# Kernel optimization log

Measured on AMD Instinct MI355X. Metric: run time of the kernel, lower is better.

## Reference

```python
import jax, jax.numpy as jnp
import numpy as np

EMB = 256
HEADS = 8

def setup_inputs() -> dict:
    key = jax.random.key(0)
    k1, k2, k3, k4, k5 = jax.random.split(key, 5)
    b, t = 8, 1024
    scale = 1.0 / np.sqrt(EMB)
    x = jax.random.normal(k1, (b, t, EMB), dtype=jnp.float32)
    # nn.Linear weights stored as [out, in]; we store [in, out] for x @ W
    Wk = jax.random.normal(k2, (EMB, EMB * HEADS), dtype=jnp.float32) * scale
    Wq = jax.random.normal(k3, (EMB, EMB * HEADS), dtype=jnp.float32) * scale
    Wv = jax.random.normal(k4, (EMB, EMB * HEADS), dtype=jnp.float32) * scale
    Wu = jax.random.normal(k5, (EMB * HEADS, EMB), dtype=jnp.float32) * scale
    return {"x": x, "Wq": Wq, "Wk": Wk, "Wv": Wv, "Wu": Wu}

def reference(x, Wq, Wk, Wv, Wu):
    b, t, e = x.shape
    h, d = HEADS, EMB  # per-head dim equals emb_in in this module
    q = (x @ Wq).reshape(b, t, h, d)
    k = (x @ Wk).reshape(b, t, h, d)
    v = (x @ Wv).reshape(b, t, h, d)
    inv4 = d ** (-0.25)
    q = q * inv4
    k = k * inv4
    # scores: [b, h, t, t]
    dot = jnp.einsum('bthd,bshd->bhts', q, k)
    attn = jax.nn.softmax(dot, axis=-1)
    out = jnp.einsum('bhts,bshd->bthd', attn, v).reshape(b, t, h * d)
    return out @ Wu
```

## Files before the change

### kernel.cpp

```cpp
#include <hip/hip_runtime.h>
#include <stdint.h>

typedef unsigned short u16;
typedef __bf16 bf16x8 __attribute__((ext_vector_type(8)));
typedef float f32x4 __attribute__((ext_vector_type(4)));
typedef u16 u16x8 __attribute__((ext_vector_type(8)));

#define MFMA16(a, b, c) __builtin_amdgcn_mfma_f32_16x16x32_bf16((a), (b), (c), 0, 0, 0)

__device__ __forceinline__ u16 f2bf(float f) {
  union { float f; uint32_t u; } v; v.f = f;
  uint32_t u = v.u;
  return (u16)((u + 0x7FFFu + ((u >> 16) & 1u)) >> 16);
}

__device__ __forceinline__ uint32_t pk2(float a, float b) {
  union { __bf16 h[2]; uint32_t u; } v;
  v.h[0] = (__bf16)a; v.h[1] = (__bf16)b;
  return v.u;
}

__device__ __forceinline__ void gload_lds16(const u16* g, u16* l) {
  __builtin_amdgcn_global_load_lds((const __attribute__((address_space(1))) void*)g,
                                   (__attribute__((address_space(3))) void*)l, 16, 0, 0);
}

__global__ void cvt_bf16(const float* __restrict__ in, u16* __restrict__ out, int n4) {
  int i = blockIdx.x * 256 + threadIdx.x;
  if (i < n4) {
    float4 v = ((const float4*)in)[i];
    ushort4 o;
    o.x = f2bf(v.x); o.y = f2bf(v.y); o.z = f2bf(v.z); o.w = f2bf(v.w);
    ((ushort4*)out)[i] = o;
  }
}

__global__ __launch_bounds__(256) void transpose_cvt(const float* __restrict__ in,
                                                     u16* __restrict__ out,
                                                     int R, int C, float scale) {
  __shared__ float t32[32][33];
  int c0 = blockIdx.x * 32, r0 = blockIdx.y * 32;
  int tx = threadIdx.x & 31, ty = threadIdx.x >> 5;
  #pragma unroll
  for (int i = 0; i < 32; i += 8)
    t32[ty + i][tx] = in[(size_t)(r0 + ty + i) * C + c0 + tx] * scale;
  __syncthreads();
  #pragma unroll
  for (int i = 0; i < 32; i += 8)
    out[(size_t)(c0 + ty + i) * R + r0 + tx] = f2bf(t32[tx][ty + i]);
}

template<int FOUT>
__global__ __launch_bounds__(256, 2) void gemm_bt(const u16* __restrict__ A,
                                                  const u16* __restrict__ Bt,
                                                  void* __restrict__ Cout,
                                                  int M, int N, int K,
                                                  int lda, int ldb, int ldc) {
  __shared__ __attribute__((aligned(16))) u16 As[128 * 32];
  __shared__ __attribute__((aligned(16))) u16 Bs[128 * 32];
  const int tid = threadIdx.x;
  const int lane = tid & 63;
  const int w = tid >> 6;
  const int wr = w >> 1, wc = w & 1;
  const int row0 = blockIdx.y * 128, col0 = blockIdx.x * 128;
  const int rr = lane & 15, kg = lane >> 4;

  f32x4 acc[4][4];
  const f32x4 fz = {0.f, 0.f, 0.f, 0.f};
  #pragma unroll
  for (int m = 0; m < 4; ++m)
    #pragma unroll
    for (int n = 0; n < 4; ++n) acc[m][n] = fz;

  for (int k0 = 0; k0 < K; k0 += 32) {
    #pragma unroll
    for (int c = 0; c < 2; ++c) {
      int Lb = c * 256 + w * 64;
      int L = Lb + lane;
      int r = L >> 2, cc = L & 3;
      gload_lds16(&A[(size_t)(row0 + r) * lda + k0 + cc * 8], &As[Lb << 3]);
      gload_lds16(&Bt[(size_t)(col0 + r) * ldb + k0 + cc * 8], &Bs[Lb << 3]);
    }
    __syncthreads();
    bf16x8 af[4], bfr[4];
    #pragma unroll
    for (int m = 0; m < 4; ++m)
      af[m] = *(const bf16x8*)&As[(wr * 64 + m * 16 + rr) * 32 + kg * 8];
    #pragma unroll
    for (int n = 0; n < 4; ++n)
      bfr[n] = *(const bf16x8*)&Bs[(wc * 64 + n * 16 + rr) * 32 + kg * 8];
    #pragma unroll
    for (int m = 0; m < 4; ++m)
      #pragma unroll
      for (int n = 0; n < 4; ++n)
        acc[m][n] = MFMA16(af[m], bfr[n], acc[m][n]);
    __syncthreads();
  }

  #pragma unroll
  for (int m = 0; m < 4; ++m)
    #pragma unroll
    for (int n = 0; n < 4; ++n) {
      int r = row0 + wr * 64 + m * 16 + kg * 4;
      int c = col0 + wc * 64 + n * 16 + rr;
      if (FOUT == 2) {
        int bb = r >> 10, tt = r & 1023;
        int hh = c >> 8, dd = c & 255;
        union { u16 h4[4]; uint2 u2; } o4;
        #pragma unroll
        for (int j = 0; j < 4; ++j) o4.h4[j] = f2bf(acc[m][n][j]);
        *(uint2*)&((u16*)Cout)[(size_t)(bb * 8 + hh) * 262144 + (size_t)dd * 1024 + tt] = o4.u2;
      } else {
        #pragma unroll
        for (int j = 0; j < 4; ++j) {
          if (FOUT == 0)
            ((u16*)Cout)[(size_t)(r + j) * ldc + c] = f2bf(acc[m][n][j]);
          else
            ((float*)Cout)[(size_t)(r + j) * ldc + c] = acc[m][n][j];
        }
      }
    }
}

template<int FOUT>
__global__ __launch_bounds__(256, 2) void gemm_bt64(const u16* __restrict__ A,
                                                    const u16* __restrict__ Bt,
                                                    void* __restrict__ Cout,
                                                    int M, int N, int K,
                                                    int lda, int ldb, int ldc) {
  __shared__ __attribute__((aligned(16))) u16 As[64 * 32];
  __shared__ __attribute__((aligned(16))) u16 Bs[128 * 32];
  const int tid = threadIdx.x;
  const int lane = tid & 63;
  const int w = tid >> 6;
  const int row0 = blockIdx.y * 64, col0 = blockIdx.x * 128;
  const int rr = lane & 15, kg = lane >> 4;

  f32x4 acc[4][2];
  const f32x4 fz = {0.f, 0.f, 0.f, 0.f};
  #pragma unroll
  for (int m = 0; m < 4; ++m)
    #pragma unroll
    for (int n = 0; n < 2; ++n) acc[m][n] = fz;

  for (int k0 = 0; k0 < K; k0 += 32) {
    {
      int Lb = w * 64;
      int L = Lb + lane;
      int r = L >> 2, cc = L & 3;
      gload_lds16(&A[(size_t)(row0 + r) * lda + k0 + cc * 8], &As[Lb << 3]);
    }
    #pragma unroll
    for (int c = 0; c < 2; ++c) {
      int Lb = c * 256 + w * 64;
      int L = Lb + lane;
      int r = L >> 2, cc = L & 3;
      gload_lds16(&Bt[(size_t)(col0 + r) * ldb + k0 + cc * 8], &Bs[Lb << 3]);
    }
    __syncthreads();
    bf16x8 af[4], bfr[2];
    #pragma unroll
    for (int m = 0; m < 4; ++m)
      af[m] = *(const bf16x8*)&As[(m * 16 + rr) * 32 + kg * 8];
    #pragma unroll
    for (int n = 0; n < 2; ++n)
      bfr[n] = *(const bf16x8*)&Bs[(w * 32 + n * 16 + rr) * 32 + kg * 8];
    #pragma unroll
    for (int m = 0; m < 4; ++m)
      #pragma unroll
      for (int n = 0; n < 2; ++n)
        acc[m][n] = MFMA16(af[m], bfr[n], acc[m][n]);
    __syncthreads();
  }

  #pragma unroll
  for (int m = 0; m < 4; ++m)
    #pragma unroll
    for (int n = 0; n < 2; ++n) {
      int r = row0 + m * 16 + kg * 4;
      int c = col0 + w * 32 + n * 16 + rr;
      #pragma unroll
      for (int j = 0; j < 4; ++j) {
        if (FOUT == 0)
          ((u16*)Cout)[(size_t)(r + j) * ldc + c] = f2bf(acc[m][n][j]);
        else
          ((float*)Cout)[(size_t)(r + j) * ldc + c] = acc[m][n][j];
      }
    }
}

__global__ __launch_bounds__(512) void attn_kernel(const u16* __restrict__ Q,
                                                   const u16* __restrict__ Kg,
                                                   const u16* __restrict__ Vt,
                                                   u16* __restrict__ O) {
  __shared__ __attribute__((aligned(16))) u16 smem[65536];
  u16* Ks = smem;
  u16* Vs = smem + 32768;
  const int tid = threadIdx.x;
  const int lane = tid & 63;
  const int w = tid >> 6;
  const int rr = lane & 15, kg = lane >> 4;
  const int bid = blockIdx.x;
  const int swz = (bid & 7) * 64 + (bid >> 3);
  const int bh = swz >> 3;
  const int b = bh >> 3, h = bh & 7;
  const int q0 = (swz & 7) * 128;
  const u16* Qb = Q + (size_t)b * 1024 * 2048 + (size_t)h * 256;
  const u16* Kb = Kg + (size_t)b * 1024 * 2048 + (size_t)h * 256;
  const u16* Vb = Vt + (size_t)bh * 262144;
  u16* Ob = O + (size_t)b * 1024 * 2048 + (size_t)h * 256;
  const int qrow = q0 + w * 16 + rr;

  auto stage_kv = [&](int sb, int s0i) {
    u16* Kd = Ks + sb * 16384;
    u16* Vd = Vs + sb * 16384;
    #pragma unroll
    for (int c = 0; c < 4; ++c) {
      int Lb = (c * 8 + w) * 64;
      int L = Lb + lane;
      int r = L >> 5, cc = L & 31;
      gload_lds16(&Kb[(size_t)(s0i + r) * 2048 + ((cc ^ (r & 7)) << 3)], &Kd[Lb << 3]);
      int rv = L >> 3, cv = L & 7;
      gload_lds16(&Vb[(size_t)rv * 1024 + s0i + ((cv ^ (rv & 7)) << 3)], &Vd[Lb << 3]);
    }
  };

  stage_kv(0, 0);

  bf16x8 qf[8];
  {
    const u16* qp = Qb + (size_t)qrow * 2048;
    #pragma unroll
    for (int kk = 0; kk < 8; ++kk) qf[kk] = *(const bf16x8*)&qp[kk * 32 + kg * 8];
  }

  const f32x4 fz = {0.f, 0.f, 0.f, 0.f};
  f32x4 oacc[16];
  #pragma unroll
  for (int dt = 0; dt < 16; ++dt) oacc[dt] = fz;
  float mrow = -1e30f, lrow = 0.f;

  __syncthreads();

  int buf = 0;
  for (int t = 0; t < 16; ++t) {
    if (t < 15) stage_kv(buf ^ 1, (t + 1) * 64);

    const u16* Kd = Ks + buf * 16384;
    f32x4 sacc[4];
    #pragma unroll
    for (int n4 = 0; n4 < 4; ++n4) sacc[n4] = fz;
    __builtin_amdgcn_s_setprio(1);
    #pragma unroll
    for (int kk = 0; kk < 8; ++kk) {
      #pragma unroll
      for (int n4 = 0; n4 < 4; ++n4) {
        int row = n4 * 16 + rr;
        int ck = kk * 4 + kg;
        bf16x8 kf = *(const bf16x8*)&Kd[row * 256 + ((ck ^ (row & 7)) << 3)];
        sacc[n4] = MFMA16(kf, qf[kk], sacc[n4]);
      }
    }
    __builtin_amdgcn_s_setprio(0);

    float vmax = sacc[0][0];
    #pragma unroll
    for (int n4 = 0; n4 < 4; ++n4)
      #pragma unroll
      for (int j = 0; j < 4; ++j) vmax = fmaxf(vmax, sacc[n4][j]);
    vmax = fmaxf(vmax, __shfl_xor(vmax, 16, 64));
    vmax = fmaxf(vmax, __shfl_xor(vmax, 32, 64));
    if (__any(vmax > mrow + 8.f)) {
      float mn = fmaxf(mrow, vmax);
      float resc = __expf(mrow - mn);
      mrow = mn;
      lrow *= resc;
      #pragma unroll
      for (int dt = 0; dt < 16; ++dt)
        #pragma unroll
        for (int i = 0; i < 4; ++i) oacc[dt][i] *= resc;
    }
    float sum = 0.f;
    uint32_t L0, H0, L1, H1, L2, H2, L3, H3;
    {
      float e0, e1, e2, e3;
      e0 = __expf(sacc[0][0] - mrow); e1 = __expf(sacc[0][1] - mrow);
      e2 = __expf(sacc[0][2] - mrow); e3 = __expf(sacc[0][3] - mrow);
      sum += (e0 + e1) + (e2 + e3); L0 = pk2(e0, e1); H0 = pk2(e2, e3);
      e0 = __expf(sacc[1][0] - mrow); e1 = __expf(sacc[1][1] - mrow);
      e2 = __expf(sacc[1][2] - mrow); e3 = __expf(sacc[1][3] - mrow);
      sum += (e0 + e1) + (e2 + e3); L1 = pk2(e0, e1); H1 = pk2(e2, e3);
      e0 = __expf(sacc[2][0] - mrow); e1 = __expf(sacc[2][1] - mrow);
      e2 = __expf(sacc[2][2] - mrow); e3 = __expf(sacc[2][3] - mrow);
      sum += (e0 + e1) + (e2 + e3); L2 = pk2(e0, e1); H2 = pk2(e2, e3);
      e0 = __expf(sacc[3][0] - mrow); e1 = __expf(sacc[3][1] - mrow);
      e2 = __expf(sacc[3][2] - mrow); e3 = __expf(sacc[3][3] - mrow);
      sum += (e0 + e1) + (e2 + e3); L3 = pk2(e0, e1); H3 = pk2(e2, e3);
    }
    sum += __shfl_xor(sum, 16, 64);
    sum += __shfl_xor(sum, 32, 64);
    lrow += sum;

    const u16* Vd = Vs + buf * 16384;
    const int g = kg;
    #pragma unroll
    for (int t2 = 0; t2 < 2; ++t2) {
      uint32_t La = t2 ? L2 : L0, Ha = t2 ? H2 : H0;
      uint32_t Lb2 = t2 ? L3 : L1, Hb = t2 ? H3 : H1;
      uint32_t La1 = __shfl_xor(La, 16, 64), La2 = __shfl_xor(La, 32, 64);
      uint32_t La3 = __shfl_xor(La1, 32, 64);
      uint32_t Ha1 = __shfl_xor(Ha, 16, 64), Ha2 = __shfl_xor(Ha, 32, 64);
      uint32_t Ha3 = __shfl_xor(Ha1, 32, 64);
      uint32_t Lb1 = __shfl_xor(Lb2, 16, 64), Lb2s = __shfl_xor(Lb2, 32, 64);
      uint32_t Lb3 = __shfl_xor(Lb1, 32, 64);
      uint32_t Hb1 = __shfl_xor(Hb, 16, 64), Hb2 = __shfl_xor(Hb, 32, 64);
      uint32_t Hb3 = __shfl_xor(Hb1, 32, 64);
      uint32_t a2S  = (g == 0) ? La  : (g == 1) ? La3 : (g == 2) ? La2 : La1;
      uint32_t a2S1 = (g == 0) ? La1 : (g == 1) ? La2 : (g == 2) ? La3 : La;
      uint32_t ah2S  = (g == 0) ? Ha  : (g == 1) ? Ha3 : (g == 2) ? Ha2 : Ha1;
      uint32_t ah2S1 = (g == 0) ? Ha1 : (g == 1) ? Ha2 : (g == 2) ? Ha3 : Ha;
      uint32_t b2S  = (g == 0) ? Lb2 : (g == 1) ? Lb3 : (g == 2) ? Lb2s : Lb1;
      uint32_t b2S1 = (g == 0) ? Lb1 : (g == 1) ? Lb2s : (g == 2) ? Lb3 : Lb2;
      uint32_t bh2S  = (g == 0) ? Hb  : (g == 1) ? Hb3 : (g == 2) ? Hb2 : Hb1;
      uint32_t bh2S1 = (g == 0) ? Hb1 : (g == 1) ? Hb2 : (g == 2) ? Hb3 : Hb;
      const int Qn = g >> 1;
      union { uint32_t u[4]; bf16x8 v; } pf;
      pf.u[0] = Qn ? b2S  : a2S;
      pf.u[1] = Qn ? bh2S : ah2S;
      pf.u[2] = Qn ? b2S1 : a2S1;
      pf.u[3] = Qn ? bh2S1 : ah2S1;
      __builtin_amdgcn_s_setprio(1);
      #pragma unroll
      for (int dt = 0; dt < 16; ++dt) {
        int rv = dt * 16 + rr;
        int cv = t2 * 4 + kg;
        bf16x8 vf = *(const bf16x8*)&Vd[rv * 64 + ((cv ^ (rv & 7)) << 3)];
        oacc[dt] = MFMA16(vf, pf.v, oacc[dt]);
      }
      __builtin_amdgcn_s_setprio(0);
    }

    __syncthreads();
    buf ^= 1;
  }

  float inv = 1.0f / lrow;
  #pragma unroll
  for (int dt = 0; dt < 16; ++dt) {
    union { u16 h4[4]; uint2 u2; } o4;
    #pragma unroll
    for (int i = 0; i < 4; ++i) o4.h4[i] = f2bf(oacc[dt][i] * inv);
    *(uint2*)&Ob[(size_t)qrow * 2048 + dt * 16 + kg * 4] = o4.u2;
  }
}

extern "C" void kernel_launch(void* const* d_in, const int* in_sizes, int n_in,
                              void* d_out, int out_size, void* d_ws, size_t ws_size,
                              hipStream_t stream) {
  const float* x  = (const float*)d_in[0];
  const float* Wq = (const float*)d_in[1];
  const float* Wk = (const float*)d_in[2];
  const float* Wv = (const float*)d_in[3];
  const float* Wu = (const float*)d_in[4];

  u16* xb  = (u16*)d_ws;
  u16* WtQ = xb  + 8192 * 256;
  u16* WtK = WtQ + 2048 * 256;
  u16* WtV = WtK + 2048 * 256;
  u16* Wut = WtV + 2048 * 256;
  u16* Qm  = Wut + 2048 * 256;
  u16* Km  = Qm  + (size_t)8192 * 2048;
  u16* Vtm = Km  + (size_t)8192 * 2048;
  u16* Om  = Vtm + (size_t)8192 * 2048;

  const float inv4 = 0.25f;

  cvt_bf16<<<2048, 256, 0, stream>>>(x, xb, 8192 * 256 / 4);
  transpose_cvt<<<dim3(64, 8), 256, 0, stream>>>(Wq, WtQ, 256, 2048, inv4);
  transpose_cvt<<<dim3(64, 8), 256, 0, stream>>>(Wk, WtK, 256, 2048, inv4);
  transpose_cvt<<<dim3(64, 8), 256, 0, stream>>>(Wv, WtV, 256, 2048, 1.0f);
  transpose_cvt<<<dim3(8, 64), 256, 0, stream>>>(Wu, Wut, 2048, 256, 1.0f);

  gemm_bt<0><<<dim3(16, 64), 256, 0, stream>>>(xb, WtQ, Qm, 8192, 2048, 256, 256, 256, 2048);
  gemm_bt<0><<<dim3(16, 64), 256, 0, stream>>>(xb, WtK, Km, 8192, 2048, 256, 256, 256, 2048);
  gemm_bt<2><<<dim3(16, 64), 256, 0, stream>>>(xb, WtV, Vtm, 8192, 2048, 256, 256, 256, 0);

  attn_kernel<<<512, 512, 0, stream>>>(Qm, Km, Vtm, Om);

  gemm_bt64<1><<<dim3(2, 128), 256, 0, stream>>>(Om, Wut, d_out, 8192, 256, 2048, 2048, 2048, 256);
}
```

Measured before the change: 215.1 us.

## Fuse QKV projections into one GEMM and process two query tiles per attention wave

The three Q/K/V projection GEMMs are merged into one launch over a concatenated 6144-column output. Each output tile routes to Q, K or the transposed V layout by column range, relying on WtQ, WtK and WtV sitting contiguously in the workspace. The attention kernel now gives each wave 32 query rows (two 16-row sets) instead of 16, so every K and V fragment read from LDS feeds two MFMAs, and the grid is halved to 256 blocks. This cuts LDS traffic and launch overhead per unit of work, but roughly doubles accumulator register use and halves the number of attention blocks, which may lower occupancy and leave CUs idle.

```diff
diff --git a/kernel.cpp b/kernel.cpp
--- a/kernel.cpp
+++ b/kernel.cpp
@@ -50,12 +50,11 @@
     out[(size_t)(c0 + ty + i) * R + r0 + tx] = f2bf(t32[tx][ty + i]);
 }
 
-template<int FOUT>
-__global__ __launch_bounds__(256, 2) void gemm_bt(const u16* __restrict__ A,
-                                                  const u16* __restrict__ Bt,
-                                                  void* __restrict__ Cout,
-                                                  int M, int N, int K,
-                                                  int lda, int ldb, int ldc) {
+__global__ __launch_bounds__(256, 2) void gemm_qkv(const u16* __restrict__ A,
+                                                   const u16* __restrict__ Bt,
+                                                   u16* __restrict__ Qm,
+                                                   u16* __restrict__ Km,
+                                                   u16* __restrict__ Vtm) {
   __shared__ __attribute__((aligned(16))) u16 As[128 * 32];
   __shared__ __attribute__((aligned(16))) u16 Bs[128 * 32];
   const int tid = threadIdx.x;
@@ -72,14 +71,14 @@
     #pragma unroll
     for (int n = 0; n < 4; ++n) acc[m][n] = fz;
 
-  for (int k0 = 0; k0 < K; k0 += 32) {
+  for (int k0 = 0; k0 < 256; k0 += 32) {
     #pragma unroll
     for (int c = 0; c < 2; ++c) {
       int Lb = c * 256 + w * 64;
       int L = Lb + lane;
       int r = L >> 2, cc = L & 3;
-      gload_lds16(&A[(size_t)(row0 + r) * lda + k0 + cc * 8], &As[Lb << 3]);
-      gload_lds16(&Bt[(size_t)(col0 + r) * ldb + k0 + cc * 8], &Bs[Lb << 3]);
+      gload_lds16(&A[(size_t)(row0 + r) * 256 + k0 + cc * 8], &As[Lb << 3]);
+      gload_lds16(&Bt[(size_t)(col0 + r) * 256 + k0 + cc * 8], &Bs[Lb << 3]);
     }
     __syncthreads();
     bf16x8 af[4], bfr[4];
@@ -103,21 +102,23 @@
     for (int n = 0; n < 4; ++n) {
       int r = row0 + wr * 64 + m * 16 + kg * 4;
       int c = col0 + wc * 64 + n * 16 + rr;
-      if (FOUT == 2) {
+      if (c < 2048) {
+        #pragma unroll
+        for (int j = 0; j < 4; ++j)
+          Qm[(size_t)(r + j) * 2048 + c] = f2bf(acc[m][n][j]);
+      } else if (c < 4096) {
+        int c2 = c - 2048;
+        #pragma unroll
+        for (int j = 0; j < 4; ++j)
+          Km[(size_t)(r + j) * 2048 + c2] = f2bf(acc[m][n][j]);
+      } else {
+        int c2 = c - 4096;
         int bb = r >> 10, tt = r & 1023;
-        int hh = c >> 8, dd = c & 255;
+        int hh = c2 >> 8, dd = c2 & 255;
         union { u16 h4[4]; uint2 u2; } o4;
         #pragma unroll
         for (int j = 0; j < 4; ++j) o4.h4[j] = f2bf(acc[m][n][j]);
-        *(uint2*)&((u16*)Cout)[(size_t)(bb * 8 + hh) * 262144 + (size_t)dd * 1024 + tt] = o4.u2;
-      } else {
-        #pragma unroll
-        for (int j = 0; j < 4; ++j) {
-          if (FOUT == 0)
-            ((u16*)Cout)[(size_t)(r + j) * ldc + c] = f2bf(acc[m][n][j]);
-          else
-            ((float*)Cout)[(size_t)(r + j) * ldc + c] = acc[m][n][j];
-        }
+        *(uint2*)&Vtm[(size_t)(bb * 8 + hh) * 262144 + (size_t)dd * 1024 + tt] = o4.u2;
       }
     }
 }
@@ -189,6 +190,49 @@
     }
 }
 
+struct PK8 { uint32_t L[4], H[4]; float sum; };
+
+__device__ __forceinline__ PK8 exppack(const f32x4* sacc, float m) {
+  PK8 r; r.sum = 0.f;
+  #pragma unroll
+  for (int n4 = 0; n4 < 4; ++n4) {
+    float e0 = __expf(sacc[n4][0] - m), e1 = __expf(sacc[n4][1] - m);
+    float e2 = __expf(sacc[n4][2] - m), e3 = __expf(sacc[n4][3] - m);
+    r.sum += (e0 + e1) + (e2 + e3);
+    r.L[n4] = pk2(e0, e1);
+    r.H[n4] = pk2(e2, e3);
+  }
+  return r;
+}
+
+__device__ __forceinline__ bf16x8 make_pf(const PK8& p, int t2, int g) {
+  uint32_t La = t2 ? p.L[2] : p.L[0], Ha = t2 ? p.H[2] : p.H[0];
+  uint32_t Lb2 = t2 ? p.L[3] : p.L[1], Hb = t2 ? p.H[3] : p.H[1];
+  uint32_t La1 = __shfl_xor(La, 16, 64), La2 = __shfl_xor(La, 32, 64);
+  uint32_t La3 = __shfl_xor(La1, 32, 64);
+  uint32_t Ha1 = __shfl_xor(Ha, 16, 64), Ha2 = __shfl_xor(Ha, 32, 64);
+  uint32_t Ha3 = __shfl_xor(Ha1, 32, 64);
+  uint32_t Lb1 = __shfl_xor(Lb2, 16, 64), Lb2s = __shfl_xor(Lb2, 32, 64);
+  uint32_t Lb3 = __shfl_xor(Lb1, 32, 64);
+  uint32_t Hb1 = __shfl_xor(Hb, 16, 64), Hb2 = __shfl_xor(Hb, 32, 64);
+  uint32_t Hb3 = __shfl_xor(Hb1, 32, 64);
+  uint32_t a2S  = (g == 0) ? La  : (g == 1) ? La3 : (g == 2) ? La2 : La1;
+  uint32_t a2S1 = (g == 0) ? La1 : (g == 1) ? La2 : (g == 2) ? La3 : La;
+  uint32_t ah2S  = (g == 0) ? Ha  : (g == 1) ? Ha3 : (g == 2) ? Ha2 : Ha1;
+  uint32_t ah2S1 = (g == 0) ? Ha1 : (g == 1) ? Ha2 : (g == 2) ? Ha3 : Ha;
+  uint32_t b2S  = (g == 0) ? Lb2 : (g == 1) ? Lb3 : (g == 2) ? Lb2s : Lb1;
+  uint32_t b2S1 = (g == 0) ? Lb1 : (g == 1) ? Lb2s : (g == 2) ? Lb3 : Lb2;
+  uint32_t bh2S  = (g == 0) ? Hb  : (g == 1) ? Hb3 : (g == 2) ? Hb2 : Hb1;
+  uint32_t bh2S1 = (g == 0) ? Hb1 : (g == 1) ? Hb2 : (g == 2) ? Hb3 : Hb;
+  const int Qn = g >> 1;
+  union { uint32_t u[4]; bf16x8 v; } pf;
+  pf.u[0] = Qn ? b2S : a2S;
+  pf.u[1] = Qn ? bh2S : ah2S;
+  pf.u[2] = Qn ? b2S1 : a2S1;
+  pf.u[3] = Qn ? bh2S1 : ah2S1;
+  return pf.v;
+}
+
 __global__ __launch_bounds__(512) void attn_kernel(const u16* __restrict__ Q,
                                                    const u16* __restrict__ Kg,
                                                    const u16* __restrict__ Vt,
@@ -201,15 +245,16 @@
   const int w = tid >> 6;
   const int rr = lane & 15, kg = lane >> 4;
   const int bid = blockIdx.x;
-  const int swz = (bid & 7) * 64 + (bid >> 3);
-  const int bh = swz >> 3;
+  const int swz = (bid & 7) * 32 + (bid >> 3);
+  const int bh = swz >> 2;
   const int b = bh >> 3, h = bh & 7;
-  const int q0 = (swz & 7) * 128;
+  const int q0 = (swz & 3) * 256;
   const u16* Qb = Q + (size_t)b * 1024 * 2048 + (size_t)h * 256;
   const u16* Kb = Kg + (size_t)b * 1024 * 2048 + (size_t)h * 256;
   const u16* Vb = Vt + (size_t)bh * 262144;
   u16* Ob = O + (size_t)b * 1024 * 2048 + (size_t)h * 256;
-  const int qrow = q0 + w * 16 + rr;
+  const int qrowA = q0 + w * 32 + rr;
+  const int qrowB = qrowA + 16;
 
   auto stage_kv = [&](int sb, int s0i) {
     u16* Kd = Ks + sb * 16384;
@@ -227,18 +272,22 @@
 
   stage_kv(0, 0);
 
-  bf16x8 qf[8];
+  bf16x8 qfA[8], qfB[8];
   {
-    const u16* qp = Qb + (size_t)qrow * 2048;
-    #pragma unroll
-    for (int kk = 0; kk < 8; ++kk) qf[kk] = *(const bf16x8*)&qp[kk * 32 + kg * 8];
+    const u16* qpA = Qb + (size_t)qrowA * 2048;
+    const u16* qpB = Qb + (size_t)qrowB * 2048;
+    #pragma unroll
+    for (int kk = 0; kk < 8; ++kk) {
+      qfA[kk] = *(const bf16x8*)&qpA[kk * 32 + kg * 8];
+      qfB[kk] = *(const bf16x8*)&qpB[kk * 32 + kg * 8];
+    }
   }
 
   const f32x4 fz = {0.f, 0.f, 0.f, 0.f};
-  f32x4 oacc[16];
-  #pragma unroll
-  for (int dt = 0; dt < 16; ++dt) oacc[dt] = fz;
-  float mrow = -1e30f, lrow = 0.f;
+  f32x4 oaccA[16], oaccB[16];
+  #pragma unroll
+  for (int dt = 0; dt < 16; ++dt) { oaccA[dt] = fz; oaccB[dt] = fz; }
+  float mrowA = -1e30f, lrowA = 0.f, mrowB = -1e30f, lrowB = 0.f;
 
   __syncthreads();
 
@@ -247,9 +296,9 @@
     if (t < 15) stage_kv(buf ^ 1, (t + 1) * 64);
 
     const u16* Kd = Ks + buf * 16384;
-    f32x4 sacc[4];
-    #pragma unroll
-    for (int n4 = 0; n4 < 4; ++n4) sacc[n4] = fz;
+    f32x4 saccA[4], saccB[4];
+    #pragma unroll
+    for (int n4 = 0; n4 < 4; ++n4) { saccA[n4] = fz; saccB[n4] = fz; }
     __builtin_amdgcn_s_setprio(1);
     #pragma unroll
     for (int kk = 0; kk < 8; ++kk) {
@@ -258,84 +307,57 @@
         int row = n4 * 16 + rr;
         int ck = kk * 4 + kg;
         bf16x8 kf = *(const bf16x8*)&Kd[row * 256 + ((ck ^ (row & 7)) << 3)];
-        sacc[n4] = MFMA16(kf, qf[kk], sacc[n4]);
+        saccA[n4] = MFMA16(kf, qfA[kk], saccA[n4]);
+        saccB[n4] = MFMA16(kf, qfB[kk], saccB[n4]);
       }
     }
     __builtin_amdgcn_s_setprio(0);
 
-    float vmax = sacc[0][0];
+    float vmaxA = saccA[0][0], vmaxB = saccB[0][0];
     #pragma unroll
     for (int n4 = 0; n4 < 4; ++n4)
       #pragma unroll
-      for (int j = 0; j < 4; ++j) vmax = fmaxf(vmax, sacc[n4][j]);
-    vmax = fmaxf(vmax, __shfl_xor(vmax, 16, 64));
-    vmax = fmaxf(vmax, __shfl_xor(vmax, 32, 64));
-    if (__any(vmax > mrow + 8.f)) {
-      float mn = fmaxf(mrow, vmax);
-      float resc = __expf(mrow - mn);
-      mrow = mn;
-      lrow *= resc;
+      for (int j = 0; j < 4; ++j) {
+        vmaxA = fmaxf(vmaxA, saccA[n4][j]);
+        vmaxB = fmaxf(vmaxB, saccB[n4][j]);
+      }
+    vmaxA = fmaxf(vmaxA, __shfl_xor(vmaxA, 16, 64));
+    vmaxA = fmaxf(vmaxA, __shfl_xor(vmaxA, 32, 64));
+    vmaxB = fmaxf(vmaxB, __shfl_xor(vmaxB, 16, 64));
+    vmaxB = fmaxf(vmaxB, __shfl_xor(vmaxB, 32, 64));
+    if (__any((vmaxA > mrowA + 8.f) || (vmaxB > mrowB + 8.f))) {
+      float mnA = fmaxf(mrowA, vmaxA), mnB = fmaxf(mrowB, vmaxB);
+      float rsA = __expf(mrowA - mnA), rsB = __expf(mrowB - mnB);
+      mrowA = mnA; mrowB = mnB;
+      lrowA *= rsA; lrowB *= rsB;
       #pragma unroll
       for (int dt = 0; dt < 16; ++dt)
         #pragma unroll
-        for (int i = 0; i < 4; ++i) oacc[dt][i] *= resc;
-    }
-    float sum = 0.f;
-    uint32_t L0, H0, L1, H1, L2, H2, L3, H3;
-    {
-      float e0, e1, e2, e3;
-      e0 = __expf(sacc[0][0] - mrow); e1 = __expf(sacc[0][1] - mrow);
-      e2 = __expf(sacc[0][2] - mrow); e3 = __expf(sacc[0][3] - mrow);
-      sum += (e0 + e1) + (e2 + e3); L0 = pk2(e0, e1); H0 = pk2(e2, e3);
-      e0 = __expf(sacc[1][0] - mrow); e1 = __expf(sacc[1][1] - mrow);
-      e2 = __expf(sacc[1][2] - mrow); e3 = __expf(sacc[1][3] - mrow);
-      sum += (e0 + e1) + (e2 + e3); L1 = pk2(e0, e1); H1 = pk2(e2, e3);
-      e0 = __expf(sacc[2][0] - mrow); e1 = __expf(sacc[2][1] - mrow);
-      e2 = __expf(sacc[2][2] - mrow); e3 = __expf(sacc[2][3] - mrow);
-      sum += (e0 + e1) + (e2 + e3); L2 = pk2(e0, e1); H2 = pk2(e2, e3);
-      e0 = __expf(sacc[3][0] - mrow); e1 = __expf(sacc[3][1] - mrow);
-      e2 = __expf(sacc[3][2] - mrow); e3 = __expf(sacc[3][3] - mrow);
-      sum += (e0 + e1) + (e2 + e3); L3 = pk2(e0, e1); H3 = pk2(e2, e3);
-    }
-    sum += __shfl_xor(sum, 16, 64);
-    sum += __shfl_xor(sum, 32, 64);
-    lrow += sum;
+        for (int i = 0; i < 4; ++i) {
+          oaccA[dt][i] *= rsA;
+          oaccB[dt][i] *= rsB;
+        }
+    }
+    PK8 pA = exppack(saccA, mrowA);
+    PK8 pB = exppack(saccB, mrowB);
+    float sA = pA.sum, sB = pB.sum;
+    sA += __shfl_xor(sA, 16, 64); sA += __shfl_xor(sA, 32, 64);
+    sB += __shfl_xor(sB, 16, 64); sB += __shfl_xor(sB, 32, 64);
+    lrowA += sA; lrowB += sB;
 
     const u16* Vd = Vs + buf * 16384;
-    const int g = kg;
     #pragma unroll
     for (int t2 = 0; t2 < 2; ++t2) {
-      uint32_t La = t2 ? L2 : L0, Ha = t2 ? H2 : H0;
-      uint32_t Lb2 = t2 ? L3 : L1, Hb = t2 ? H3 : H1;
-      uint32_t La1 = __shfl_xor(La, 16, 64), La2 = __shfl_xor(La, 32, 64);
-      uint32_t La3 = __shfl_xor(La1, 32, 64);
-      uint32_t Ha1 = __shfl_xor(Ha, 16, 64), Ha2 = __shfl_xor(Ha, 32, 64);
-      uint32_t Ha3 = __shfl_xor(Ha1, 32, 64);
-      uint32_t Lb1 = __shfl_xor(Lb2, 16, 64), Lb2s = __shfl_xor(Lb2, 32, 64);
-      uint32_t Lb3 = __shfl_xor(Lb1, 32, 64);
-      uint32_t Hb1 = __shfl_xor(Hb, 16, 64), Hb2 = __shfl_xor(Hb, 32, 64);
-      uint32_t Hb3 = __shfl_xor(Hb1, 32, 64);
-      uint32_t a2S  = (g == 0) ? La  : (g == 1) ? La3 : (g == 2) ? La2 : La1;
-      uint32_t a2S1 = (g == 0) ? La1 : (g == 1) ? La2 : (g == 2) ? La3 : La;
-      uint32_t ah2S  = (g == 0) ? Ha  : (g == 1) ? Ha3 : (g == 2) ? Ha2 : Ha1;
-      uint32_t ah2S1 = (g == 0) ? Ha1 : (g == 1) ? Ha2 : (g == 2) ? Ha3 : Ha;
-      uint32_t b2S  = (g == 0) ? Lb2 : (g == 1) ? Lb3 : (g == 2) ? Lb2s : Lb1;
-      uint32_t b2S1 = (g == 0) ? Lb1 : (g == 1) ? Lb2s : (g == 2) ? Lb3 : Lb2;
-      uint32_t bh2S  = (g == 0) ? Hb  : (g == 1) ? Hb3 : (g == 2) ? Hb2 : Hb1;
-      uint32_t bh2S1 = (g == 0) ? Hb1 : (g == 1) ? Hb2 : (g == 2) ? Hb3 : Hb;
-      const int Qn = g >> 1;
-      union { uint32_t u[4]; bf16x8 v; } pf;
-      pf.u[0] = Qn ? b2S  : a2S;
-      pf.u[1] = Qn ? bh2S : ah2S;
-      pf.u[2] = Qn ? b2S1 : a2S1;
-      pf.u[3] = Qn ? bh2S1 : ah2S1;
+      bf16x8 pfA = make_pf(pA, t2, kg);
+      bf16x8 pfB = make_pf(pB, t2, kg);
       __builtin_amdgcn_s_setprio(1);
       #pragma unroll
       for (int dt = 0; dt < 16; ++dt) {
         int rv = dt * 16 + rr;
         int cv = t2 * 4 + kg;
         bf16x8 vf = *(const bf16x8*)&Vd[rv * 64 + ((cv ^ (rv & 7)) << 3)];
-        oacc[dt] = MFMA16(vf, pf.v, oacc[dt]);
+        oaccA[dt] = MFMA16(vf, pfA, oaccA[dt]);
+        oaccB[dt] = MFMA16(vf, pfB, oaccB[dt]);
       }
       __builtin_amdgcn_s_setprio(0);
     }
@@ -344,13 +366,17 @@
     buf ^= 1;
   }
 
-  float inv = 1.0f / lrow;
+  float invA = 1.0f / lrowA, invB = 1.0f / lrowB;
   #pragma unroll
   for (int dt = 0; dt < 16; ++dt) {
-    union { u16 h4[4]; uint2 u2; } o4;
-    #pragma unroll
-    for (int i = 0; i < 4; ++i) o4.h4[i] = f2bf(oacc[dt][i] * inv);
-    *(uint2*)&Ob[(size_t)qrow * 2048 + dt * 16 + kg * 4] = o4.u2;
+    union { u16 h4[4]; uint2 u2; } oA, oB;
+    #pragma unroll
+    for (int i = 0; i < 4; ++i) {
+      oA.h4[i] = f2bf(oaccA[dt][i] * invA);
+      oB.h4[i] = f2bf(oaccB[dt][i] * invB);
+    }
+    *(uint2*)&Ob[(size_t)qrowA * 2048 + dt * 16 + kg * 4] = oA.u2;
+    *(uint2*)&Ob[(size_t)qrowB * 2048 + dt * 16 + kg * 4] = oB.u2;
   }
 }
 
@@ -381,11 +407,9 @@
   transpose_cvt<<<dim3(64, 8), 256, 0, stream>>>(Wv, WtV, 256, 2048, 1.0f);
   transpose_cvt<<<dim3(8, 64), 256, 0, stream>>>(Wu, Wut, 2048, 256, 1.0f);
 
-  gemm_bt<0><<<dim3(16, 64), 256, 0, stream>>>(xb, WtQ, Qm, 8192, 2048, 256, 256, 256, 2048);
-  gemm_bt<0><<<dim3(16, 64), 256, 0, stream>>>(xb, WtK, Km, 8192, 2048, 256, 256, 256, 2048);
-  gemm_bt<2><<<dim3(16, 64), 256, 0, stream>>>(xb, WtV, Vtm, 8192, 2048, 256, 256, 256, 0);
-
-  attn_kernel<<<512, 512, 0, stream>>>(Qm, Km, Vtm, Om);
+  gemm_qkv<<<dim3(48, 64), 256, 0, stream>>>(xb, WtQ, Qm, Km, Vtm);
+
+  attn_kernel<<<256, 512, 0, stream>>>(Qm, Km, Vtm, Om);
 
   gemm_bt64<1><<<dim3(2, 128), 256, 0, stream>>>(Om, Wut, d_out, 8192, 256, 2048, 2048, 2048, 256);
 }
```

After: 216.8 us. About the same (+0.8%).
